# Kernel tuning notes

Hardware: AMD Instinct MI355X
Metric: run time of the kernel (lower is better)

Reference implementation:

```python
import jax, jax.numpy as jnp
import numpy as np

NUM_EMBEDDINGS = 512
EMBEDDING_DIM = 128
COMMITMENT_COST = 0.25


def setup_inputs() -> dict:
    key = jax.random.key(0)
    k1, k2 = jax.random.split(key)
    inputs = jax.random.normal(k1, (8, EMBEDDING_DIM, 32, 32, 32), dtype=jnp.float32)
    limit = 1.0 / NUM_EMBEDDINGS
    weight = jax.random.uniform(k2, (NUM_EMBEDDINGS, EMBEDDING_DIM), dtype=jnp.float32,
                                minval=-limit, maxval=limit)
    return {"inputs": inputs, "weight": weight}


def reference(inputs, weight):
    sg = jax.lax.stop_gradient
    # (B, C, D, H, W) -> (B, D, H, W, C)
    x = jnp.transpose(inputs, (0, 2, 3, 4, 1))
    C = x.shape[-1]
    flat = x.reshape(-1, C)  # [N, C]
    distances = (jnp.sum(flat * flat, axis=1, keepdims=True)
                 + jnp.sum(weight * weight, axis=1)
                 - 2.0 * flat @ weight.T)
    encoding_indices = jnp.argmin(distances, axis=1)  # [N]
    encodings = jax.nn.one_hot(encoding_indices, weight.shape[0], dtype=jnp.float32)  # [N, E]
    # gather is mathematically identical to encodings @ weight
    quantized = weight[encoding_indices].reshape(x.shape)
    e_latent_loss = jnp.mean((sg(quantized) - x) ** 2)
    q_latent_loss = jnp.mean((quantized - sg(x)) ** 2)
    loss = q_latent_loss + COMMITMENT_COST * e_latent_loss
    # straight-through estimator
    quantized_st = x + sg(quantized - x)
    avg_probs = jnp.mean(encodings, axis=0)
    perplexity = jnp.exp(-jnp.sum(avg_probs * jnp.log(avg_probs + 1e-10)))
    out_q = jnp.transpose(quantized_st, (0, 4, 1, 2, 3))  # back to (B, C, D, H, W)
    return loss, out_q, perplexity, encodings
```

## Files before the change

### kernel.cpp

```cpp
#include <hip/hip_runtime.h>
#include <math.h>

#define CDIM 128
#define EDIM 512
#define BLK 256
#define MT 64
#define ECH 64
#define NVEC 262144
#define SPATIAL 32768
#define QELEMS 33554432LL
#define TIE_T 4e-6f

typedef __bf16 bf16x8 __attribute__((ext_vector_type(8)));
typedef float  f32x4  __attribute__((ext_vector_type(4)));

struct WS {
  float  wnh[EDIM];
  int    counts[EDIM];
  double lossAcc;
  double _pad;
  unsigned int wp[EDIM * CDIM];
};

__device__ inline unsigned short f2bf(float f) {
  unsigned u = __float_as_uint(f);
  return (unsigned short)((u + 0x7fffu + ((u >> 16) & 1u)) >> 16);
}
__device__ inline float bf2f(unsigned short h) {
  return __uint_as_float(((unsigned)h) << 16);
}

__global__ __launch_bounds__(512) void vq_pre(const float* __restrict__ wt,
                                              WS* __restrict__ ws, int buildWP) {
  int t = threadIdx.x;
  const float* w = wt + (size_t)t * CDIM;
  float a0 = 0.f, a1 = 0.f, a2 = 0.f, a3 = 0.f;
#pragma unroll
  for (int c = 0; c < CDIM; c += 4) {
    a0 = fmaf(w[c + 0], w[c + 0], a0);
    a1 = fmaf(w[c + 1], w[c + 1], a1);
    a2 = fmaf(w[c + 2], w[c + 2], a2);
    a3 = fmaf(w[c + 3], w[c + 3], a3);
  }
  ws->wnh[t] = 0.5f * ((a0 + a1) + (a2 + a3));
  ws->counts[t] = 0;
  if (t == 0) ws->lossAcc = 0.0;
  if (buildWP) {
    for (int c = 0; c < CDIM; ++c) {
      float f = w[c];
      unsigned short h = f2bf(f);
      unsigned short l = f2bf(f - bf2f(h));
      ws->wp[(size_t)t * CDIM + c] = (((unsigned)h) << 16) | (unsigned)l;
    }
  }
}

__device__ double score64(const float* __restrict__ in, const float* __restrict__ wt,
                          size_t xoff, int e) {
  const float* w = wt + (size_t)e * CDIM;
  double a = 0.0;
  for (int c = 0; c < CDIM; ++c) {
    double wd = (double)w[c];
    double xv = (double)in[xoff + (size_t)c * SPATIAL];
    a = fma(wd, fma(0.5, wd, -xv), a);
  }
  return a;
}


template <bool USEWP>
__global__ __launch_bounds__(BLK, 2) void vq_main(const float* __restrict__ in,
                                                  const float* __restrict__ wt,
                                                  WS* __restrict__ ws,
                                                  float* __restrict__ out_q,
                                                  float* __restrict__ enc) {
  __shared__ __align__(16) unsigned short xhi[4 * 2176];
  __shared__ __align__(16) unsigned short xlo[4 * 2176];
  __shared__ __align__(16) char wuni[2 * ECH * 136 * 2];
  __shared__ float  wn_l[EDIM];
  __shared__ int    hist[EDIM];
  __shared__ int    sIdx[MT];
  __shared__ double lred[BLK];

  unsigned short* whl = (unsigned short*)wuni;
  unsigned short* wll = whl + ECH * 136;

  const int tid = threadIdx.x;
  for (int e = tid; e < EDIM; e += BLK) { wn_l[e] = ws->wnh[e]; hist[e] = 0; }

  const int n0 = blockIdx.x * MT;
  const int b  = n0 >> 15;
  const int s0 = n0 & (SPATIAL - 1);
  const size_t ibase = (size_t)b * CDIM * SPATIAL;

  {
    const int mq = tid & 15;
    const int cr = tid >> 4;
    const int m0 = mq * 4;
#pragma unroll
    for (int p = 0; p < 8; ++p) {
      int c = cr + p * 16;
      float4 v = *(const float4*)(in + ibase + (size_t)c * SPATIAL + s0 + m0);
      int sb = (m0 >> 4) * 2176 + (c >> 3) * 136 + (m0 & 15) * 8 + (c & 7);
#pragma unroll
      for (int i = 0; i < 4; ++i) {
        float f = ((const float*)&v)[i];
        unsigned short h = f2bf(f);
        unsigned short l = f2bf(f - bf2f(h));
        xhi[sb + i * 8] = h;
        xlo[sb + i * 8] = l;
      }
    }
  }

  const int lane = tid & 63, wv = tid >> 6;
  const int col = lane & 15, g = lane >> 4;

  float b1[4], b2[4], b3[4]; int i1[4], i2[4];
#pragma unroll
  for (int i = 0; i < 4; ++i) { b1[i] = 1e30f; b2[i] = 1e30f; b3[i] = 1e30f; i1[i] = 0; i2[i] = 0; }

  for (int ch = 0; ch < 8; ++ch) {
    const int e0c = ch * ECH;
    __syncthreads();
    if (USEWP) {
      const uint4* wp4 = (const uint4*)(ws->wp + (size_t)e0c * CDIM);
#pragma unroll
      for (int i = 0; i < 8; ++i) {
        int q = i * BLK + tid;
        int e = q >> 5, k0 = (q & 31) * 4;
        uint4 W = wp4[q];
        unsigned hi01 = __builtin_amdgcn_perm(W.y, W.x, 0x07060302u);
        unsigned lo01 = __builtin_amdgcn_perm(W.y, W.x, 0x05040100u);
        unsigned hi23 = __builtin_amdgcn_perm(W.w, W.z, 0x07060302u);
        unsigned lo23 = __builtin_amdgcn_perm(W.w, W.z, 0x05040100u);
        *(uint2*)&whl[e * 136 + k0] = make_uint2(hi01, hi23);
        *(uint2*)&wll[e * 136 + k0] = make_uint2(lo01, lo23);
      }
    } else {
      const float* wbase = wt + (size_t)e0c * CDIM;
#pragma unroll
      for (int i = 0; i < 8; ++i) {
        int q = i * BLK + tid;
        int e = q >> 5, k0 = (q & 31) * 4;
        float4 F = *(const float4*)(wbase + (size_t)e * CDIM + k0);
        unsigned short h0 = f2bf(F.x), h1 = f2bf(F.y), h2 = f2bf(F.z), h3 = f2bf(F.w);
        unsigned short l0 = f2bf(F.x - bf2f(h0)), l1 = f2bf(F.y - bf2f(h1));
        unsigned short l2 = f2bf(F.z - bf2f(h2)), l3 = f2bf(F.w - bf2f(h3));
        *(uint2*)&whl[e * 136 + k0] =
            make_uint2((unsigned)h0 | ((unsigned)h1 << 16), (unsigned)h2 | ((unsigned)h3 << 16));
        *(uint2*)&wll[e * 136 + k0] =
            make_uint2((unsigned)l0 | ((unsigned)l1 << 16), (unsigned)l2 | ((unsigned)l3 << 16));
      }
    }
    __syncthreads();

    bf16x8 ah[4], al[4];
#pragma unroll
    for (int kt = 0; kt < 4; ++kt) {
      int rowb = (wv * 16 + col) * 136 + kt * 32 + g * 8;
      ah[kt] = *(const bf16x8*)&whl[rowb];
      al[kt] = *(const bf16x8*)&wll[rowb];
    }

    f32x4 acc[4];
#pragma unroll
    for (int mt = 0; mt < 4; ++mt) {
      f32x4 a = {0.f, 0.f, 0.f, 0.f};
#pragma unroll
      for (int kt = 0; kt < 4; ++kt) {
        int xb = mt * 2176 + (kt * 4 + g) * 136 + col * 8;
        bf16x8 bh = *(const bf16x8*)&xhi[xb];
        bf16x8 bl = *(const bf16x8*)&xlo[xb];
        a = __builtin_amdgcn_mfma_f32_16x16x32_bf16(ah[kt], bh, a, 0, 0, 0);
        a = __builtin_amdgcn_mfma_f32_16x16x32_bf16(ah[kt], bl, a, 0, 0, 0);
        a = __builtin_amdgcn_mfma_f32_16x16x32_bf16(al[kt], bh, a, 0, 0, 0);
        a = __builtin_amdgcn_mfma_f32_16x16x32_bf16(al[kt], bl, a, 0, 0, 0);
      }
      acc[mt] = a;
    }

    const int e0 = e0c + wv * 16 + g * 4;
    float4 wn = *(const float4*)&wn_l[e0];
#pragma unroll
    for (int mt = 0; mt < 4; ++mt) {
#pragma unroll
      for (int r = 0; r < 4; ++r) {
        float sc = ((const float*)&wn)[r] - acc[mt][r];
        int e = e0 + r;
        if (sc < b1[mt]) { b3[mt] = b2[mt]; b2[mt] = b1[mt]; i2[mt] = i1[mt]; b1[mt] = sc; i1[mt] = e; }
        else if (sc < b2[mt]) { b3[mt] = b2[mt]; b2[mt] = sc; i2[mt] = e; }
        else if (sc < b3[mt]) { b3[mt] = sc; }
      }
    }
  }

  __syncthreads();
  float (*cb1)[17] = (float(*)[17])wuni;
  float (*cb2)[17] = (float(*)[17])(wuni + 4352);
  float (*cb3)[17] = (float(*)[17])(wuni + 8704);
  int   (*ci1)[17] = (int(*)[17])(wuni + 13056);
  int   (*ci2)[17] = (int(*)[17])(wuni + 17408);

#pragma unroll
  for (int mt = 0; mt < 4; ++mt) {
    int m = mt * 16 + col, slot = wv * 4 + g;
    cb1[m][slot] = b1[mt]; cb2[m][slot] = b2[mt]; cb3[m][slot] = b3[mt];
    ci1[m][slot] = i1[mt]; ci2[m][slot] = i2[mt];
  }
  __syncthreads();

  if (tid < MT) {
    const int vec = tid;
    float m1 = 1e30f, m2 = 1e30f, m3 = 1e30f;
    int j1 = 0x7fffffff, j2 = 0x7fffffff;
    auto ins = [&](float v, int ix) {
      bool q1 = (v < m1) || (v == m1 && ix < j1);
      bool q2 = (v < m2) || (v == m2 && ix < j2);
      if (q1)      { m3 = m2; m2 = m1; j2 = j1; m1 = v; j1 = ix; }
      else if (q2) { m3 = m2; m2 = v; j2 = ix; }
      else if (v < m3) { m3 = v; }
    };
    for (int t = 0; t < 16; ++t) {
      ins(cb1[vec][t], ci1[vec][t]);
      ins(cb2[vec][t], ci2[vec][t]);
      ins(cb3[vec][t], 0x7fffffff);
    }
    int bi = j1;
    const size_t xoff = ibase + s0 + vec;
    if (m3 - m1 < TIE_T) {
      double bd = 1e300; int bj = 0;
      for (int e = 0; e < EDIM; ++e) {
        double a = score64(in, wt, xoff, e);
        if (a < bd) { bd = a; bj = e; }
      }
      bi = bj;
    } else if (m2 - m1 < TIE_T) {
      double s1 = score64(in, wt, xoff, j1);
      double s2 = score64(in, wt, xoff, j2);
      if (s2 < s1 || (s2 == s1 && j2 < j1)) bi = j2;
    }
    sIdx[vec] = bi;
    atomicAdd(&hist[bi], 1);
  }
  __syncthreads();

  {
    const int vec = tid & (MT - 1);
    const int qd  = tid >> 6;
    const int bi  = sIdx[vec];
    const float* wq = wt + (size_t)bi * CDIM;
    const size_t gbase = ibase + s0 + vec;
    double ls = 0.0;
#pragma unroll
    for (int cc = 0; cc < 32; cc += 4) {
      int c = qd * 32 + cc;
      int eb = (vec >> 4) * 2176 + (c >> 3) * 136 + (vec & 15) * 8 + (c & 7);
      uint2 hq = *(const uint2*)&xhi[eb];
      uint2 lq = *(const uint2*)&xlo[eb];
      float xs0 = bf2f((unsigned short)(hq.x & 0xffffu)) + bf2f((unsigned short)(lq.x & 0xffffu));
      float xs1 = bf2f((unsigned short)(hq.x >> 16))     + bf2f((unsigned short)(lq.x >> 16));
      float xs2 = bf2f((unsigned short)(hq.y & 0xffffu)) + bf2f((unsigned short)(lq.y & 0xffffu));
      float xs3 = bf2f((unsigned short)(hq.y >> 16))     + bf2f((unsigned short)(lq.y >> 16));
      float4 qv = *(const float4*)(wq + c);
      __builtin_nontemporal_store(qv.x, out_q + gbase + (size_t)(c + 0) * SPATIAL);
      __builtin_nontemporal_store(qv.y, out_q + gbase + (size_t)(c + 1) * SPATIAL);
      __builtin_nontemporal_store(qv.z, out_q + gbase + (size_t)(c + 2) * SPATIAL);
      __builtin_nontemporal_store(qv.w, out_q + gbase + (size_t)(c + 3) * SPATIAL);
      double d0 = (double)qv.x - (double)xs0; ls = fma(d0, d0, ls);
      double d1 = (double)qv.y - (double)xs1; ls = fma(d1, d1, ls);
      double d2 = (double)qv.z - (double)xs2; ls = fma(d2, d2, ls);
      double d3 = (double)qv.w - (double)xs3; ls = fma(d3, d3, ls);
    }
    lred[tid] = ls;
  }
  __syncthreads();
  for (int off = BLK / 2; off > 0; off >>= 1) {
    if (tid < off) lred[tid] += lred[tid + off];
    __syncthreads();
  }
  if (tid == 0) atomicAdd(&ws->lossAcc, lred[0]);

  {
    const size_t r0 = (size_t)blockIdx.x * MT;
    const int c0 = tid * 2;
    unsigned long long* e2 = (unsigned long long*)enc;
    for (int r = 0; r < MT; ++r) {
      int idx = sIdx[r];
      union { float2 f; unsigned long long u; } cvt;
      cvt.f.x = (idx == c0) ? 1.0f : 0.0f;
      cvt.f.y = (idx == c0 + 1) ? 1.0f : 0.0f;
      __builtin_nontemporal_store(cvt.u, e2 + (r0 + (size_t)r) * (EDIM / 2) + tid);
    }
  }

  for (int e = tid; e < EDIM; e += BLK) {
    int v = hist[e];
    if (v) atomicAdd(&ws->counts[e], v);
  }
}

__global__ __launch_bounds__(512) void vq_fin(const WS* __restrict__ ws, float* __restrict__ out) {
  __shared__ double red[EDIM];
  int t = threadIdx.x;
  double p = (double)ws->counts[t] * (1.0 / (double)NVEC);
  red[t] = p * log(p + 1e-10);
  __syncthreads();
  for (int off = 256; off > 0; off >>= 1) {
    if (t < off) red[t] += red[t + off];
    __syncthreads();
  }
  if (t == 0) {
    out[0] = (float)(1.25 * ws->lossAcc / (double)QELEMS);
    out[1 + QELEMS] = (float)exp(-red[0]);
  }
}

extern "C" void kernel_launch(void* const* d_in, const int* in_sizes, int n_in,
                              void* d_out, int out_size, void* d_ws, size_t ws_size,
                              hipStream_t stream) {
  const float* in = (const float*)d_in[0];
  const float* wt = (const float*)d_in[1];
  float* out = (float*)d_out;
  WS* ws = (WS*)d_ws;

  float* out_q = out + 1;
  float* enc   = out + 2 + QELEMS;

  const bool useWP = (ws_size >= sizeof(WS));
  vq_pre<<<dim3(1), dim3(512), 0, stream>>>(wt, ws, useWP ? 1 : 0);
  if (useWP)
    vq_main<true><<<dim3(NVEC / MT), dim3(BLK), 0, stream>>>(in, wt, ws, out_q, enc);
  else
    vq_main<false><<<dim3(NVEC / MT), dim3(BLK), 0, stream>>>(in, wt, ws, out_q, enc);
  vq_fin<<<dim3(1), dim3(512), 0, stream>>>(ws, out);
}
```

Before: 1.045 ms.

## Load pre-swizzled codebook fragments from global memory and drop the lo×lo MFMA

The codebook is now pre-split into bf16 hi/lo arrays, stored in MFMA fragment order by a parallelised 64-block pre-kernel. Each wave loads its A fragments straight from global/L2 rather than staging them through LDS behind per-chunk barriers. The lo×lo MFMA term is dropped, cutting matrix work by a quarter at a small precision cost that the fp64 rescoring of the top-2 candidates is meant to absorb. LDS use shrinks to allow 4 blocks per CU, a swizzled x layout replaces padding, top-3 merging uses shuffles, loss reduction uses wave shuffles, and histogram counts use global atomics directly.

After: 1.275 ms. 22.1% more time.

```diff
diff --git a/kernel.cpp b/kernel.cpp
--- a/kernel.cpp
+++ b/kernel.cpp
@@ -5,7 +5,6 @@
 #define EDIM 512
 #define BLK 256
 #define MT 64
-#define ECH 64
 #define NVEC 262144
 #define SPATIAL 32768
 #define QELEMS 33554432LL
@@ -19,39 +18,52 @@
   int    counts[EDIM];
   double lossAcc;
   double _pad;
-  unsigned int wp[EDIM * CDIM];
+  unsigned short wph[EDIM * CDIM];
+  unsigned short wpl[EDIM * CDIM];
 };
 
-__device__ inline unsigned short f2bf(float f) {
-  unsigned u = __float_as_uint(f);
-  return (unsigned short)((u + 0x7fffu + ((u >> 16) & 1u)) >> 16);
-}
-__device__ inline float bf2f(unsigned short h) {
-  return __uint_as_float(((unsigned)h) << 16);
-}
-
-__global__ __launch_bounds__(512) void vq_pre(const float* __restrict__ wt,
+__device__ inline unsigned short bfbits(float f) {
+  union { __bf16 b; unsigned short u; } cv; cv.b = (__bf16)f; return cv.u;
+}
+__device__ inline void split2(float x0, float x1, unsigned& hv, unsigned& lv) {
+  unsigned short h0 = bfbits(x0), h1 = bfbits(x1);
+  float r0 = x0 - __uint_as_float((unsigned)h0 << 16);
+  float r1 = x1 - __uint_as_float((unsigned)h1 << 16);
+  unsigned short l0 = bfbits(r0), l1 = bfbits(r1);
+  hv = (unsigned)h0 | ((unsigned)h1 << 16);
+  lv = (unsigned)l0 | ((unsigned)l1 << 16);
+}
+
+__device__ inline void ins3(float v, int ix, float& m1, float& m2, float& m3,
+                            int& j1, int& j2) {
+  bool q1 = (v < m1) || (v == m1 && ix < j1);
+  bool q2 = (v < m2) || (v == m2 && ix < j2);
+  if (q1)      { m3 = m2; m2 = m1; j2 = j1; m1 = v; j1 = ix; }
+  else if (q2) { m3 = m2; m2 = v; j2 = ix; }
+  else if (v < m3) { m3 = v; }
+}
+
+__global__ __launch_bounds__(256) void vq_pre(const float* __restrict__ wt,
                                               WS* __restrict__ ws, int buildWP) {
-  int t = threadIdx.x;
-  const float* w = wt + (size_t)t * CDIM;
-  float a0 = 0.f, a1 = 0.f, a2 = 0.f, a3 = 0.f;
-#pragma unroll
-  for (int c = 0; c < CDIM; c += 4) {
-    a0 = fmaf(w[c + 0], w[c + 0], a0);
-    a1 = fmaf(w[c + 1], w[c + 1], a1);
-    a2 = fmaf(w[c + 2], w[c + 2], a2);
-    a3 = fmaf(w[c + 3], w[c + 3], a3);
-  }
-  ws->wnh[t] = 0.5f * ((a0 + a1) + (a2 + a3));
-  ws->counts[t] = 0;
-  if (t == 0) ws->lossAcc = 0.0;
+  const int tid = threadIdx.x, bid = blockIdx.x;
+  const int e = bid * 8 + (tid >> 5);
+  const int k0 = (tid & 31) * 4;
+  float4 F = *(const float4*)(wt + (size_t)e * CDIM + k0);
+  float nrm = F.x * F.x + F.y * F.y + F.z * F.z + F.w * F.w;
+#pragma unroll
+  for (int off = 1; off < 32; off <<= 1) nrm += __shfl_xor(nrm, off);
+  if ((tid & 31) == 0) ws->wnh[e] = 0.5f * nrm;
+  if (tid < 8) ws->counts[bid * 8 + tid] = 0;
+  if (bid == 0 && tid == 0) ws->lossAcc = 0.0;
   if (buildWP) {
-    for (int c = 0; c < CDIM; ++c) {
-      float f = w[c];
-      unsigned short h = f2bf(f);
-      unsigned short l = f2bf(f - bf2f(h));
-      ws->wp[(size_t)t * CDIM + c] = (((unsigned)h) << 16) | (unsigned)l;
-    }
+    const int etile = e >> 4, row = e & 15;
+    const int kt = k0 >> 5, g = (k0 >> 3) & 3, j0 = k0 & 7;
+    size_t idx = ((size_t)(etile * 4 + kt) * 64 + g * 16 + row) * 8 + j0;
+    unsigned hv0, lv0, hv1, lv1;
+    split2(F.x, F.y, hv0, lv0);
+    split2(F.z, F.w, hv1, lv1);
+    *(uint2*)&ws->wph[idx] = make_uint2(hv0, hv1);
+    *(uint2*)&ws->wpl[idx] = make_uint2(lv0, lv1);
   }
 }
 
@@ -67,27 +79,20 @@
   return a;
 }
 
-
 template <bool USEWP>
-__global__ __launch_bounds__(BLK, 2) void vq_main(const float* __restrict__ in,
+__global__ __launch_bounds__(BLK, 4) void vq_main(const float* __restrict__ in,
                                                   const float* __restrict__ wt,
                                                   WS* __restrict__ ws,
                                                   float* __restrict__ out_q,
                                                   float* __restrict__ enc) {
-  __shared__ __align__(16) unsigned short xhi[4 * 2176];
-  __shared__ __align__(16) unsigned short xlo[4 * 2176];
-  __shared__ __align__(16) char wuni[2 * ECH * 136 * 2];
-  __shared__ float  wn_l[EDIM];
-  __shared__ int    hist[EDIM];
+  __shared__ __align__(16) unsigned short xhi[8192];
+  __shared__ __align__(16) unsigned short xlo[8192];
+  __shared__ float cb1[MT][5], cb2[MT][5], cb3[MT][5];
+  __shared__ int   ci1[MT][5], ci2[MT][5];
   __shared__ int    sIdx[MT];
-  __shared__ double lred[BLK];
-
-  unsigned short* whl = (unsigned short*)wuni;
-  unsigned short* wll = whl + ECH * 136;
+  __shared__ double lredw[4];
 
   const int tid = threadIdx.x;
-  for (int e = tid; e < EDIM; e += BLK) { wn_l[e] = ws->wnh[e]; hist[e] = 0; }
-
   const int n0 = blockIdx.x * MT;
   const int b  = n0 >> 15;
   const int s0 = n0 & (SPATIAL - 1);
@@ -95,72 +100,62 @@
 
   {
     const int mq = tid & 15;
-    const int cr = tid >> 4;
-    const int m0 = mq * 4;
-#pragma unroll
-    for (int p = 0; p < 8; ++p) {
-      int c = cr + p * 16;
-      float4 v = *(const float4*)(in + ibase + (size_t)c * SPATIAL + s0 + m0);
-      int sb = (m0 >> 4) * 2176 + (c >> 3) * 136 + (m0 & 15) * 8 + (c & 7);
-#pragma unroll
-      for (int i = 0; i < 4; ++i) {
-        float f = ((const float*)&v)[i];
-        unsigned short h = f2bf(f);
-        unsigned short l = f2bf(f - bf2f(h));
-        xhi[sb + i * 8] = h;
-        xlo[sb + i * 8] = l;
-      }
-    }
-  }
+    const int cg = tid >> 4;
+    const int m0 = mq * 4, c0 = cg * 8;
+    float4 F[8];
+#pragma unroll
+    for (int i = 0; i < 8; ++i)
+      F[i] = *(const float4*)(in + ibase + (size_t)(c0 + i) * SPATIAL + s0 + m0);
+#pragma unroll
+    for (int mi = 0; mi < 4; ++mi) {
+      const int m = m0 + mi;
+      unsigned hv[4], lv[4];
+#pragma unroll
+      for (int p = 0; p < 4; ++p)
+        split2(((const float*)&F[2 * p])[mi], ((const float*)&F[2 * p + 1])[mi],
+               hv[p], lv[p]);
+      const int fm = (m & 15) ^ ((m & 15) >> 2);
+      const int elem = cg * 512 + (m >> 4) * 128 + fm * 8;
+      *(uint4*)&xhi[elem] = make_uint4(hv[0], hv[1], hv[2], hv[3]);
+      *(uint4*)&xlo[elem] = make_uint4(lv[0], lv[1], lv[2], lv[3]);
+    }
+  }
+  __syncthreads();
 
   const int lane = tid & 63, wv = tid >> 6;
   const int col = lane & 15, g = lane >> 4;
+  const int fcol = col ^ (col >> 2);
 
   float b1[4], b2[4], b3[4]; int i1[4], i2[4];
 #pragma unroll
   for (int i = 0; i < 4; ++i) { b1[i] = 1e30f; b2[i] = 1e30f; b3[i] = 1e30f; i1[i] = 0; i2[i] = 0; }
 
   for (int ch = 0; ch < 8; ++ch) {
-    const int e0c = ch * ECH;
-    __syncthreads();
+    const int etile = ch * 4 + wv;
+    bf16x8 ah[4], al[4];
     if (USEWP) {
-      const uint4* wp4 = (const uint4*)(ws->wp + (size_t)e0c * CDIM);
-#pragma unroll
-      for (int i = 0; i < 8; ++i) {
-        int q = i * BLK + tid;
-        int e = q >> 5, k0 = (q & 31) * 4;
-        uint4 W = wp4[q];
-        unsigned hi01 = __builtin_amdgcn_perm(W.y, W.x, 0x07060302u);
-        unsigned lo01 = __builtin_amdgcn_perm(W.y, W.x, 0x05040100u);
-        unsigned hi23 = __builtin_amdgcn_perm(W.w, W.z, 0x07060302u);
-        unsigned lo23 = __builtin_amdgcn_perm(W.w, W.z, 0x05040100u);
-        *(uint2*)&whl[e * 136 + k0] = make_uint2(hi01, hi23);
-        *(uint2*)&wll[e * 136 + k0] = make_uint2(lo01, lo23);
+#pragma unroll
+      for (int kt = 0; kt < 4; ++kt) {
+        size_t aoff = ((size_t)(etile * 4 + kt) * 64 + lane) * 8;
+        ah[kt] = *(const bf16x8*)&ws->wph[aoff];
+        al[kt] = *(const bf16x8*)&ws->wpl[aoff];
       }
     } else {
-      const float* wbase = wt + (size_t)e0c * CDIM;
-#pragma unroll
-      for (int i = 0; i < 8; ++i) {
-        int q = i * BLK + tid;
-        int e = q >> 5, k0 = (q & 31) * 4;
-        float4 F = *(const float4*)(wbase + (size_t)e * CDIM + k0);
-        unsigned short h0 = f2bf(F.x), h1 = f2bf(F.y), h2 = f2bf(F.z), h3 = f2bf(F.w);
-        unsigned short l0 = f2bf(F.x - bf2f(h0)), l1 = f2bf(F.y - bf2f(h1));
-        unsigned short l2 = f2bf(F.z - bf2f(h2)), l3 = f2bf(F.w - bf2f(h3));
-        *(uint2*)&whl[e * 136 + k0] =
-            make_uint2((unsigned)h0 | ((unsigned)h1 << 16), (unsigned)h2 | ((unsigned)h3 << 16));
-        *(uint2*)&wll[e * 136 + k0] =
-            make_uint2((unsigned)l0 | ((unsigned)l1 << 16), (unsigned)l2 | ((unsigned)l3 << 16));
-      }
-    }
-    __syncthreads();
-
-    bf16x8 ah[4], al[4];
-#pragma unroll
-    for (int kt = 0; kt < 4; ++kt) {
-      int rowb = (wv * 16 + col) * 136 + kt * 32 + g * 8;
-      ah[kt] = *(const bf16x8*)&whl[rowb];
-      al[kt] = *(const bf16x8*)&wll[rowb];
+      const int e = etile * 16 + col;
+#pragma unroll
+      for (int kt = 0; kt < 4; ++kt) {
+        const float* wp = wt + (size_t)e * CDIM + kt * 32 + g * 8;
+        float4 Fa = *(const float4*)wp, Fb = *(const float4*)(wp + 4);
+        float xf[8] = {Fa.x, Fa.y, Fa.z, Fa.w, Fb.x, Fb.y, Fb.z, Fb.w};
+        bf16x8 h, l;
+#pragma unroll
+        for (int j = 0; j < 8; ++j) {
+          __bf16 hb = (__bf16)xf[j];
+          float r = xf[j] - (float)hb;
+          h[j] = hb; l[j] = (__bf16)r;
+        }
+        ah[kt] = h; al[kt] = l;
+      }
     }
 
     f32x4 acc[4];
@@ -169,62 +164,60 @@
       f32x4 a = {0.f, 0.f, 0.f, 0.f};
 #pragma unroll
       for (int kt = 0; kt < 4; ++kt) {
-        int xb = mt * 2176 + (kt * 4 + g) * 136 + col * 8;
+        const int xb = (kt * 4 + g) * 512 + mt * 128 + fcol * 8;
         bf16x8 bh = *(const bf16x8*)&xhi[xb];
         bf16x8 bl = *(const bf16x8*)&xlo[xb];
         a = __builtin_amdgcn_mfma_f32_16x16x32_bf16(ah[kt], bh, a, 0, 0, 0);
         a = __builtin_amdgcn_mfma_f32_16x16x32_bf16(ah[kt], bl, a, 0, 0, 0);
         a = __builtin_amdgcn_mfma_f32_16x16x32_bf16(al[kt], bh, a, 0, 0, 0);
-        a = __builtin_amdgcn_mfma_f32_16x16x32_bf16(al[kt], bl, a, 0, 0, 0);
       }
       acc[mt] = a;
     }
 
-    const int e0 = e0c + wv * 16 + g * 4;
-    float4 wn = *(const float4*)&wn_l[e0];
+    const int e0 = ch * 64 + wv * 16 + g * 4;
+    const float4 wn = *(const float4*)&ws->wnh[e0];
 #pragma unroll
     for (int mt = 0; mt < 4; ++mt) {
 #pragma unroll
       for (int r = 0; r < 4; ++r) {
         float sc = ((const float*)&wn)[r] - acc[mt][r];
-        int e = e0 + r;
-        if (sc < b1[mt]) { b3[mt] = b2[mt]; b2[mt] = b1[mt]; i2[mt] = i1[mt]; b1[mt] = sc; i1[mt] = e; }
-        else if (sc < b2[mt]) { b3[mt] = b2[mt]; b2[mt] = sc; i2[mt] = e; }
-        else if (sc < b3[mt]) { b3[mt] = sc; }
-      }
-    }
-  }
-
-  __syncthreads();
-  float (*cb1)[17] = (float(*)[17])wuni;
-  float (*cb2)[17] = (float(*)[17])(wuni + 4352);
-  float (*cb3)[17] = (float(*)[17])(wuni + 8704);
-  int   (*ci1)[17] = (int(*)[17])(wuni + 13056);
-  int   (*ci2)[17] = (int(*)[17])(wuni + 17408);
+        ins3(sc, e0 + r, b1[mt], b2[mt], b3[mt], i1[mt], i2[mt]);
+      }
+    }
+  }
 
 #pragma unroll
   for (int mt = 0; mt < 4; ++mt) {
-    int m = mt * 16 + col, slot = wv * 4 + g;
-    cb1[m][slot] = b1[mt]; cb2[m][slot] = b2[mt]; cb3[m][slot] = b3[mt];
-    ci1[m][slot] = i1[mt]; ci2[m][slot] = i2[mt];
+#pragma unroll
+    for (int sh = 0; sh < 2; ++sh) {
+      const int off = 16 << sh;
+      float p1 = __shfl_xor(b1[mt], off), p2 = __shfl_xor(b2[mt], off),
+            p3 = __shfl_xor(b3[mt], off);
+      int q1 = __shfl_xor(i1[mt], off), q2 = __shfl_xor(i2[mt], off);
+      ins3(p1, q1, b1[mt], b2[mt], b3[mt], i1[mt], i2[mt]);
+      ins3(p2, q2, b1[mt], b2[mt], b3[mt], i1[mt], i2[mt]);
+      ins3(p3, 0x7fffffff, b1[mt], b2[mt], b3[mt], i1[mt], i2[mt]);
+    }
+  }
+  if (g == 0) {
+#pragma unroll
+    for (int mt = 0; mt < 4; ++mt) {
+      const int m = mt * 16 + col;
+      cb1[m][wv] = b1[mt]; cb2[m][wv] = b2[mt]; cb3[m][wv] = b3[mt];
+      ci1[m][wv] = i1[mt]; ci2[m][wv] = i2[mt];
+    }
   }
   __syncthreads();
 
   if (tid < MT) {
     const int vec = tid;
-    float m1 = 1e30f, m2 = 1e30f, m3 = 1e30f;
-    int j1 = 0x7fffffff, j2 = 0x7fffffff;
-    auto ins = [&](float v, int ix) {
-      bool q1 = (v < m1) || (v == m1 && ix < j1);
-      bool q2 = (v < m2) || (v == m2 && ix < j2);
-      if (q1)      { m3 = m2; m2 = m1; j2 = j1; m1 = v; j1 = ix; }
-      else if (q2) { m3 = m2; m2 = v; j2 = ix; }
-      else if (v < m3) { m3 = v; }
-    };
-    for (int t = 0; t < 16; ++t) {
-      ins(cb1[vec][t], ci1[vec][t]);
-      ins(cb2[vec][t], ci2[vec][t]);
-      ins(cb3[vec][t], 0x7fffffff);
+    float m1 = cb1[vec][0], m2 = cb2[vec][0], m3 = cb3[vec][0];
+    int j1 = ci1[vec][0], j2 = ci2[vec][0];
+#pragma unroll
+    for (int t = 1; t < 4; ++t) {
+      ins3(cb1[vec][t], ci1[vec][t], m1, m2, m3, j1, j2);
+      ins3(cb2[vec][t], ci2[vec][t], m1, m2, m3, j1, j2);
+      ins3(cb3[vec][t], 0x7fffffff, m1, m2, m3, j1, j2);
     }
     int bi = j1;
     const size_t xoff = ibase + s0 + vec;
@@ -241,7 +234,7 @@
       if (s2 < s1 || (s2 == s1 && j2 < j1)) bi = j2;
     }
     sIdx[vec] = bi;
-    atomicAdd(&hist[bi], 1);
+    atomicAdd(&ws->counts[bi], 1);
   }
   __syncthreads();
 
@@ -251,17 +244,18 @@
     const int bi  = sIdx[vec];
     const float* wq = wt + (size_t)bi * CDIM;
     const size_t gbase = ibase + s0 + vec;
+    const int fv = (vec & 15) ^ ((vec & 15) >> 2);
     double ls = 0.0;
 #pragma unroll
     for (int cc = 0; cc < 32; cc += 4) {
-      int c = qd * 32 + cc;
-      int eb = (vec >> 4) * 2176 + (c >> 3) * 136 + (vec & 15) * 8 + (c & 7);
-      uint2 hq = *(const uint2*)&xhi[eb];
-      uint2 lq = *(const uint2*)&xlo[eb];
-      float xs0 = bf2f((unsigned short)(hq.x & 0xffffu)) + bf2f((unsigned short)(lq.x & 0xffffu));
-      float xs1 = bf2f((unsigned short)(hq.x >> 16))     + bf2f((unsigned short)(lq.x >> 16));
-      float xs2 = bf2f((unsigned short)(hq.y & 0xffffu)) + bf2f((unsigned short)(lq.y & 0xffffu));
-      float xs3 = bf2f((unsigned short)(hq.y >> 16))     + bf2f((unsigned short)(lq.y >> 16));
+      const int c = qd * 32 + cc;
+      const int elem = (c >> 3) * 512 + (vec >> 4) * 128 + fv * 8 + (c & 7);
+      uint2 hq = *(const uint2*)&xhi[elem];
+      uint2 lq = *(const uint2*)&xlo[elem];
+      float xs0 = __uint_as_float(hq.x << 16)        + __uint_as_float(lq.x << 16);
+      float xs1 = __uint_as_float(hq.x & 0xffff0000u) + __uint_as_float(lq.x & 0xffff0000u);
+      float xs2 = __uint_as_float(hq.y << 16)        + __uint_as_float(lq.y << 16);
+      float xs3 = __uint_as_float(hq.y & 0xffff0000u) + __uint_as_float(lq.y & 0xffff0000u);
       float4 qv = *(const float4*)(wq + c);
       __builtin_nontemporal_store(qv.x, out_q + gbase + (size_t)(c + 0) * SPATIAL);
       __builtin_nontemporal_store(qv.y, out_q + gbase + (size_t)(c + 1) * SPATIAL);
@@ -272,14 +266,12 @@
       double d2 = (double)qv.z - (double)xs2; ls = fma(d2, d2, ls);
       double d3 = (double)qv.w - (double)xs3; ls = fma(d3, d3, ls);
     }
-    lred[tid] = ls;
-  }
-  __syncthreads();
-  for (int off = BLK / 2; off > 0; off >>= 1) {
-    if (tid < off) lred[tid] += lred[tid + off];
-    __syncthreads();
-  }
-  if (tid == 0) atomicAdd(&ws->lossAcc, lred[0]);
+#pragma unroll
+    for (int off = 32; off > 0; off >>= 1) ls += __shfl_down(ls, off);
+    if (lane == 0) lredw[wv] = ls;
+  }
+  __syncthreads();
+  if (tid == 0) atomicAdd(&ws->lossAcc, lredw[0] + lredw[1] + lredw[2] + lredw[3]);
 
   {
     const size_t r0 = (size_t)blockIdx.x * MT;
@@ -293,11 +285,6 @@
       __builtin_nontemporal_store(cvt.u, e2 + (r0 + (size_t)r) * (EDIM / 2) + tid);
     }
   }
-
-  for (int e = tid; e < EDIM; e += BLK) {
-    int v = hist[e];
-    if (v) atomicAdd(&ws->counts[e], v);
-  }
 }
 
 __global__ __launch_bounds__(512) void vq_fin(const WS* __restrict__ ws, float* __restrict__ out) {
@@ -328,7 +315,7 @@
   float* enc   = out + 2 + QELEMS;
 
   const bool useWP = (ws_size >= sizeof(WS));
-  vq_pre<<<dim3(1), dim3(512), 0, stream>>>(wt, ws, useWP ? 1 : 0);
+  vq_pre<<<dim3(64), dim3(256), 0, stream>>>(wt, ws, useWP ? 1 : 0);
   if (useWP)
     vq_main<true><<<dim3(NVEC / MT), dim3(BLK), 0, stream>>>(in, wt, ws, out_q, enc);
   else
```
